# Kernel optimization log

Measured on AMD Instinct MI355X. Metric: run time of the kernel, lower is better.

The kernel has to match this reference:

```python
import jax, jax.numpy as jnp
import numpy as np

B, D, H = 16384, 1024, 1024
EPS = 1e-07


def setup_inputs() -> dict:
    key = jax.random.key(0)
    ks = jax.random.split(key, 16)
    s = 1.0 / np.sqrt(D)  # xavier-ish scale keeps exp() gate bounded
    mat = lambda k: (jax.random.normal(k, (D, H), dtype=jnp.float32) * s)
    zeros = lambda: jnp.zeros((H,), dtype=jnp.float32)
    return {
        "x": jax.random.normal(ks[0], (B, D), dtype=jnp.float32),
        "h_prev": jax.random.normal(ks[1], (B, H), dtype=jnp.float32) * 0.1,
        "c_prev": jax.random.normal(ks[2], (B, H), dtype=jnp.float32) * 0.1,
        "n_prev": jnp.ones((B, H), dtype=jnp.float32),
        "Wz": mat(ks[3]), "bWz": zeros(), "Rz": mat(ks[4]), "bRz": zeros(), "bz": zeros(),
        "Wi": mat(ks[5]), "bWi": zeros(), "Ri": mat(ks[6]), "bRi": zeros(), "bi": zeros(),
        "Wf": mat(ks[7]), "bWf": zeros(), "Rf": mat(ks[8]), "bRf": zeros(), "bf": zeros(),
        "Wo": mat(ks[9]), "bWo": zeros(), "Ro": mat(ks[10]), "bRo": zeros(), "bo": zeros(),
        "Wy": mat(ks[11]), "by": jnp.zeros((D,), dtype=jnp.float32),
    }


def reference(x, h_prev, c_prev, n_prev,
              Wz, bWz, Rz, bRz, bz,
              Wi, bWi, Ri, bRi, bi,
              Wf, bWf, Rf, bRf, bf,
              Wo, bWo, Ro, bRo, bo,
              Wy, by):
    # pre-activations: two fused GEMMs via concatenated weights
    Wcat = jnp.concatenate([Wz, Wi, Wf, Wo], axis=1)      # [D, 4H]
    Rcat = jnp.concatenate([Rz, Ri, Rf, Ro], axis=1)      # [H, 4H]
    bcat = jnp.concatenate([bWz + bRz + bz, bWi + bRi + bi,
                            bWf + bRf + bf, bWo + bRo + bo])
    pre = x @ Wcat + h_prev @ Rcat + bcat                  # [B, 4H]
    pz, pi, pf, po = jnp.split(pre, 4, axis=1)
    zt = jnp.tanh(pz)
    it = jnp.exp(pi)
    ft = jax.nn.sigmoid(pf)
    ot = jax.nn.sigmoid(po)
    C = ft * c_prev + it * zt
    n = ft * n_prev + it
    h = ot * jnp.tanh(C / (n + EPS))
    y = h @ Wy + by
    return y, (h, C, n)
```

## Files before the change

### kernel.cpp

```cpp
#include <hip/hip_runtime.h>
#include <math.h>
#include <stdint.h>


typedef __attribute__((ext_vector_type(8))) short bf16x8;
typedef __attribute__((ext_vector_type(4))) float f32x4;

constexpr int Bsz = 16384;
constexpr int Dd  = 1024;
constexpr int Hh  = 1024;
constexpr float EPSv = 1e-7f;

__device__ __forceinline__ unsigned short f2bf(float f) {
    union { float f; uint32_t u; } v; v.f = f;
    uint32_t u = v.u + 0x7fffu + ((v.u >> 16) & 1u);
    return (unsigned short)(u >> 16);
}

__device__ __forceinline__ void gload16(const void* g, void* l) {
    __builtin_amdgcn_global_load_lds(
        (const __attribute__((address_space(1))) void*)g,
        (__attribute__((address_space(3))) void*)l, 16, 0, 0);
}

__device__ __forceinline__ float sigm_f(float x) { return 1.f / (1.f + __expf(-x)); }
__device__ __forceinline__ float tanh_f(float x) {
    const float ax = fabsf(x);
    const float t = __expf(-2.f * ax);
    const float r = (1.f - t) / (1.f + t);
    return copysignf(r, x);
}

#define DSR(d, a, o) asm volatile("ds_read_b128 %0, %1 offset:" o : "=v"(d) : "v"(a) : "memory")

struct CvtArgs {
    const float* x;
    const float* hp;
    unsigned short* abf;
    const float* src[9];
    const float* bptr[12];
    unsigned short* wt;
    unsigned short* wyt;
    float* bs;
};

__global__ __launch_bounds__(256)
void cvt_all(CvtArgs P)
{
    __shared__ float tile[64][65];
    const int bid = blockIdx.x;
    const int t = threadIdx.x;

    if (bid < 16384) {
        const int idx = bid * 256 + t;
        const int n = idx * 8;
        const int b = n >> 11, k = n & 2047;
        const float* s = (k < 1024) ? (P.x + (size_t)b * 1024 + k)
                                    : (P.hp + (size_t)b * 1024 + (k - 1024));
        const float4 v0 = *(const float4*)s;
        const float4 v1 = *(const float4*)(s + 4);
        union { unsigned short u[8]; uint4 v; } pk;
        pk.u[0] = f2bf(v0.x); pk.u[1] = f2bf(v0.y); pk.u[2] = f2bf(v0.z); pk.u[3] = f2bf(v0.w);
        pk.u[4] = f2bf(v1.x); pk.u[5] = f2bf(v1.y); pk.u[6] = f2bf(v1.z); pk.u[7] = f2bf(v1.w);
        *(uint4*)(P.abf + n) = pk.v;
        return;
    }
    if (bid >= 18688) {
        const int j = (bid - 18688) * 256 + t;
        P.bs[j]        = P.bptr[0][j] + P.bptr[1][j]  + P.bptr[2][j];
        P.bs[1024 + j] = P.bptr[3][j] + P.bptr[4][j]  + P.bptr[5][j];
        P.bs[2048 + j] = P.bptr[6][j] + P.bptr[7][j]  + P.bptr[8][j];
        P.bs[3072 + j] = P.bptr[9][j] + P.bptr[10][j] + P.bptr[11][j];
        return;
    }
    const int wb = bid - 16384;
    const int id = wb >> 8, sub = wb & 255;
    const float* __restrict__ src = P.src[id];
    const int kt = sub & 15, jt = sub >> 4;
    {
        const int lr = t >> 4, lc = (t & 15) * 4;
        #pragma unroll
        for (int rr = 0; rr < 64; rr += 16) {
            const float4 v = *(const float4*)(src + (size_t)(kt * 64 + rr + lr) * 1024 + jt * 64 + lc);
            tile[rr + lr][lc + 0] = v.x;
            tile[rr + lr][lc + 1] = v.y;
            tile[rr + lr][lc + 2] = v.z;
            tile[rr + lr][lc + 3] = v.w;
        }
    }
    __syncthreads();
    const int jl = t >> 2, kc = (t & 3) * 16;
    const int j = jt * 64 + jl;
    union { unsigned short u[16]; uint4 v[2]; } pk;
    #pragma unroll
    for (int q = 0; q < 16; ++q) pk.u[q] = f2bf(tile[kc + q][jl]);
    uint4* d;
    if (id == 8) {
        d = (uint4*)(P.wyt + (size_t)j * 1024 + kt * 64 + kc);
    } else {
        const int g = id >> 1, kbase = (id & 1) ? 1024 : 0;
        const int cp = (j & 15) | (g << 4) | ((j >> 4) << 6);
        d = (uint4*)(P.wt + (size_t)cp * 2048 + kbase + kt * 64 + kc);
    }
    d[0] = pk.v[0];
    d[1] = pk.v[1];
}


template<int LD, int NTK, int NTILES, class Epi>
__device__ void mfma_core(const unsigned short* __restrict__ Ag,
                          const unsigned short* __restrict__ Bg,
                          int m0base, int n0, int t,
                          unsigned short* lds, Epi epi)
{
    constexpr int TOT = NTK * NTILES;
    const int lane = t & 63, wid = t >> 6;
    const int wr = wid >> 2, wc = wid & 3;
    const int cl = lane & 15, hi = lane >> 4;
    const int Lb = (int)(size_t)(__attribute__((address_space(3))) unsigned short*)lds;
    const int rdA0 = Lb + (wr * 128 + cl) * 128 + ((hi ^ (cl & 7)) << 4);
    const int rdB0 = Lb + 65536 + (wc * 64 + cl) * 128 + ((hi ^ (cl & 7)) << 4);
    const int srow = t >> 3;
    const int schk = ((t & 7) ^ (srow & 7)) * 8;
    const int sdst = t * 16;
    char* const L = (char*)lds;

    auto stgA = [&](int f, int buf) {
        const int ot = f / NTK, kt = f % NTK;
        const unsigned short* g = Ag + (size_t)(m0base + ot * 256 + srow) * LD + kt * 64 + schk;
        char* d = L + buf * 32768 + sdst;
        gload16(g,                  d);
        gload16(g + (size_t) 64 * LD, d + 8192);
        gload16(g + (size_t)128 * LD, d + 16384);
        gload16(g + (size_t)192 * LD, d + 24576);
    };
    auto stgB = [&](int f, int buf) {
        const int kt = f % NTK;
        const unsigned short* g = Bg + (size_t)(n0 + srow) * LD + kt * 64 + schk;
        char* d = L + 65536 + buf * 32768 + sdst;
        gload16(g,                  d);
        gload16(g + (size_t) 64 * LD, d + 8192);
        gload16(g + (size_t)128 * LD, d + 16384);
        gload16(g + (size_t)192 * LD, d + 24576);
    };

    f32x4 acc[8][4];
    #pragma unroll
    for (int i = 0; i < 8; ++i)
        #pragma unroll
        for (int j = 0; j < 4; ++j) acc[i][j] = (f32x4)0.f;

    stgA(0, 0); stgB(0, 0); stgB(1, 1);

    int bA = 0, bB = 0;
    for (int f = 0; f < TOT; ++f) {
        const int f1 = (f + 1 < TOT) ? f + 1 : TOT - 1;
        const int f2 = (f + 2 < TOT) ? f + 2 : TOT - 1;
        const int bB2 = (bB >= 1) ? bB - 1 : 2;

        asm volatile("s_waitcnt vmcnt(4)" ::: "memory");
        __builtin_amdgcn_s_barrier();
        stgA(f1, bA ^ 1);
        stgB(f2, bB2);

        const int aof  = rdA0 + (bA << 15);
        const int bof  = rdB0 + (bB << 15);
        const int aof1 = aof ^ 64;
        const int bof1 = bof ^ 64;
        bf16x8 a0[8], b0[4], a1[8], b1[4];

        DSR(a0[0], aof, "0");     DSR(a0[1], aof, "2048");
        DSR(a0[2], aof, "4096");  DSR(a0[3], aof, "6144");
        DSR(a0[4], aof, "8192");  DSR(a0[5], aof, "10240");
        DSR(a0[6], aof, "12288"); DSR(a0[7], aof, "14336");
        DSR(b0[0], bof, "0");     DSR(b0[1], bof, "2048");
        DSR(b0[2], bof, "4096");  DSR(b0[3], bof, "6144");
        DSR(a1[0], aof1, "0");     DSR(a1[1], aof1, "2048");
        DSR(a1[2], aof1, "4096");  DSR(a1[3], aof1, "6144");
        DSR(a1[4], aof1, "8192");  DSR(a1[5], aof1, "10240");
        DSR(a1[6], aof1, "12288"); DSR(a1[7], aof1, "14336");

        asm volatile("s_waitcnt lgkmcnt(8)" ::: "memory");
        __builtin_amdgcn_sched_barrier(0);
        __builtin_amdgcn_s_setprio(1);
        #pragma unroll
        for (int mf = 0; mf < 8; ++mf)
            #pragma unroll
            for (int nf = 0; nf < 4; ++nf)
                acc[mf][nf] = __builtin_amdgcn_mfma_f32_16x16x32_bf16(a0[mf], b0[nf], acc[mf][nf], 0, 0, 0);

        DSR(b1[0], bof1, "0");    DSR(b1[1], bof1, "2048");
        DSR(b1[2], bof1, "4096"); DSR(b1[3], bof1, "6144");

        asm volatile("s_waitcnt lgkmcnt(0)" ::: "memory");
        __builtin_amdgcn_sched_barrier(0);
        #pragma unroll
        for (int mf = 0; mf < 8; ++mf)
            #pragma unroll
            for (int nf = 0; nf < 4; ++nf)
                acc[mf][nf] = __builtin_amdgcn_mfma_f32_16x16x32_bf16(a1[mf], b1[nf], acc[mf][nf], 0, 0, 0);
        __builtin_amdgcn_s_setprio(0);

        if ((f % NTK) == NTK - 1) {
            epi(f / NTK, acc);
            #pragma unroll
            for (int i = 0; i < 8; ++i)
                #pragma unroll
                for (int j = 0; j < 4; ++j) acc[i][j] = (f32x4)0.f;
        }
        bA ^= 1;
        bB = (bB == 2) ? 0 : bB + 1;
    }
    asm volatile("s_waitcnt vmcnt(0)" ::: "memory");
}

__global__ __launch_bounds__(512, 2)
void gemm_gates(const unsigned short* __restrict__ A, const unsigned short* __restrict__ WT,
                const float* __restrict__ bsum,
                const float* __restrict__ c_prev, const float* __restrict__ n_prev,
                float* __restrict__ out_h, float* __restrict__ out_C, float* __restrict__ out_n,
                unsigned short* __restrict__ h_bf)
{
    __shared__ unsigned short lds[81920];
    const int t = threadIdx.x;
    const int b = blockIdx.x;
    const int nb  = (b & 7) * 2 + (b >> 7);
    const int mb0 = ((b >> 3) & 15) * 4;
    const int m0base = mb0 * 256;
    const int n0 = nb * 256;

    const int lane = t & 63, wid = t >> 6;
    const int wr = wid >> 2, wc = wid & 3;
    const int cl = lane & 15, hi = lane >> 4;
    const int j_out = nb * 64 + wc * 16 + cl;
    const float bz_ = bsum[j_out];
    const float bi_ = bsum[1024 + j_out];
    const float bf_ = bsum[2048 + j_out];
    const float bo_ = bsum[3072 + j_out];

    auto epi = [&](int ot, f32x4 (&acc)[8][4]) {
        #pragma unroll
        for (int mf = 0; mf < 8; ++mf) {
            const int rb = m0base + ot * 256 + wr * 128 + mf * 16 + hi * 4;
            #pragma unroll
            for (int r = 0; r < 4; ++r) {
                const size_t idx = (size_t)(rb + r) * 1024 + j_out;
                const float pz = acc[mf][0][r] + bz_;
                const float pi = acc[mf][1][r] + bi_;
                const float pf = acc[mf][2][r] + bf_;
                const float po = acc[mf][3][r] + bo_;
                const float zt = tanh_f(pz);
                const float it = __expf(pi);
                const float ft = sigm_f(pf);
                const float ot_ = sigm_f(po);
                const float Cv = ft * c_prev[idx] + it * zt;
                const float nv = ft * n_prev[idx] + it;
                const float hv = ot_ * tanh_f(Cv / (nv + EPSv));
                __builtin_nontemporal_store(hv, &out_h[idx]);
                __builtin_nontemporal_store(Cv, &out_C[idx]);
                __builtin_nontemporal_store(nv, &out_n[idx]);
                h_bf[idx] = f2bf(hv);
            }
        }
    };

    mfma_core<2048, 32, 4>(A, WT, m0base, n0, t, lds, epi);
}

__global__ __launch_bounds__(512, 2)
void gemm_y(const unsigned short* __restrict__ A, const unsigned short* __restrict__ WyT,
            const float* __restrict__ by, float* __restrict__ y)
{
    __shared__ unsigned short lds[81920];
    const int t = threadIdx.x;
    const int b = blockIdx.x;
    const int nb = b & 3, mb = b >> 2;
    const int m0base = mb * 256, n0 = nb * 256;

    const int lane = t & 63, wid = t >> 6;
    const int wr = wid >> 2, wc = wid & 3;
    const int cl = lane & 15, hi = lane >> 4;

    auto epi = [&](int ot, f32x4 (&acc)[8][4]) {
        (void)ot;
        #pragma unroll
        for (int mf = 0; mf < 8; ++mf) {
            const int rb = m0base + wr * 128 + mf * 16 + hi * 4;
            #pragma unroll
            for (int nf = 0; nf < 4; ++nf) {
                const int c = n0 + wc * 64 + nf * 16 + cl;
                const float bc = by[c];
                #pragma unroll
                for (int r = 0; r < 4; ++r)
                    __builtin_nontemporal_store(acc[mf][nf][r] + bc, &y[(size_t)(rb + r) * 1024 + c]);
            }
        }
    };

    mfma_core<1024, 16, 1>(A, WyT, m0base, n0, t, lds, epi);
}


constexpr int FBM = 64, FBN = 64, FBK = 16, FPAD = 4;

__global__ __launch_bounds__(256)
void fb_gates(const float* __restrict__ x, const float* __restrict__ h_prev,
              const float* __restrict__ c_prev, const float* __restrict__ n_prev,
              const float* __restrict__ Wz, const float* __restrict__ Rz,
              const float* __restrict__ Wi, const float* __restrict__ Ri,
              const float* __restrict__ Wf, const float* __restrict__ Rf,
              const float* __restrict__ Wo, const float* __restrict__ Ro,
              const float* __restrict__ bWz, const float* __restrict__ bRz, const float* __restrict__ bz,
              const float* __restrict__ bWi, const float* __restrict__ bRi, const float* __restrict__ bi,
              const float* __restrict__ bWf, const float* __restrict__ bRf, const float* __restrict__ bf_,
              const float* __restrict__ bWo, const float* __restrict__ bRo, const float* __restrict__ bo,
              float* __restrict__ out_h, float* __restrict__ out_C, float* __restrict__ out_n)
{
    __shared__ float sA[FBK][FBM + FPAD];
    __shared__ float sB[4][FBK][FBN + FPAD];
    const int t = threadIdx.x;
    const int col_blk = blockIdx.x & 15, row_blk = blockIdx.x >> 4;
    const int row0 = row_blk * FBM, col0 = col_blk * FBN;
    const int tx = t & 15, ty = t >> 4;
    float acc[4][4][4];
    #pragma unroll
    for (int g = 0; g < 4; ++g)
        for (int i = 0; i < 4; ++i)
            for (int j = 0; j < 4; ++j) acc[g][i][j] = 0.f;
    const int ar = t >> 2, ak = (t & 3) * 4, wk = t >> 4, wcc = (t & 15) * 4;
    for (int phase = 0; phase < 2; ++phase) {
        const float* Am = phase ? h_prev : x;
        const float* W0 = phase ? Rz : Wz; const float* W1 = phase ? Ri : Wi;
        const float* W2 = phase ? Rf : Wf; const float* W3 = phase ? Ro : Wo;
        for (int k0 = 0; k0 < 1024; k0 += FBK) {
            __syncthreads();
            {
                const float4 v = *(const float4*)(Am + (size_t)(row0 + ar) * 1024 + k0 + ak);
                sA[ak + 0][ar] = v.x; sA[ak + 1][ar] = v.y;
                sA[ak + 2][ar] = v.z; sA[ak + 3][ar] = v.w;
            }
            *(float4*)&sB[0][wk][wcc] = *(const float4*)(W0 + (size_t)(k0 + wk) * 1024 + col0 + wcc);
            *(float4*)&sB[1][wk][wcc] = *(const float4*)(W1 + (size_t)(k0 + wk) * 1024 + col0 + wcc);
            *(float4*)&sB[2][wk][wcc] = *(const float4*)(W2 + (size_t)(k0 + wk) * 1024 + col0 + wcc);
            *(float4*)&sB[3][wk][wcc] = *(const float4*)(W3 + (size_t)(k0 + wk) * 1024 + col0 + wcc);
            __syncthreads();
            #pragma unroll
            for (int kk = 0; kk < FBK; ++kk) {
                float a[4], bb[4][4];
                *(float4*)a = *(const float4*)&sA[kk][ty * 4];
                *(float4*)&bb[0][0] = *(const float4*)&sB[0][kk][tx * 4];
                *(float4*)&bb[1][0] = *(const float4*)&sB[1][kk][tx * 4];
                *(float4*)&bb[2][0] = *(const float4*)&sB[2][kk][tx * 4];
                *(float4*)&bb[3][0] = *(const float4*)&sB[3][kk][tx * 4];
                #pragma unroll
                for (int g = 0; g < 4; ++g)
                    for (int i = 0; i < 4; ++i)
                        for (int j = 0; j < 4; ++j)
                            acc[g][i][j] += a[i] * bb[g][j];
            }
        }
    }
    #pragma unroll
    for (int i = 0; i < 4; ++i) {
        const int r = row0 + ty * 4 + i;
        #pragma unroll
        for (int j = 0; j < 4; ++j) {
            const int c = col0 + tx * 4 + j;
            const float pz = acc[0][i][j] + bWz[c] + bRz[c] + bz[c];
            const float pi = acc[1][i][j] + bWi[c] + bRi[c] + bi[c];
            const float pf = acc[2][i][j] + bWf[c] + bRf[c] + bf_[c];
            const float po = acc[3][i][j] + bWo[c] + bRo[c] + bo[c];
            const float zt = tanhf(pz);
            const float it = expf(pi);
            const float ft = 1.f / (1.f + expf(-pf));
            const float ot = 1.f / (1.f + expf(-po));
            const size_t idx = (size_t)r * Hh + c;
            const float Cv = ft * c_prev[idx] + it * zt;
            const float nv = ft * n_prev[idx] + it;
            out_h[idx] = ot * tanhf(Cv / (nv + EPSv));
            out_C[idx] = Cv;
            out_n[idx] = nv;
        }
    }
}

__global__ __launch_bounds__(256)
void fb_ygemm(const float* __restrict__ hmat, const float* __restrict__ Wy,
              const float* __restrict__ by, float* __restrict__ y)
{
    __shared__ float sA[FBK][FBM + FPAD];
    __shared__ float sB[FBK][FBN + FPAD];
    const int t = threadIdx.x;
    const int col_blk = blockIdx.x & 15, row_blk = blockIdx.x >> 4;
    const int row0 = row_blk * FBM, col0 = col_blk * FBN;
    const int tx = t & 15, ty = t >> 4;
    float acc[4][4];
    #pragma unroll
    for (int i = 0; i < 4; ++i)
        for (int j = 0; j < 4; ++j) acc[i][j] = 0.f;
    const int ar = t >> 2, ak = (t & 3) * 4, wk = t >> 4, wcc = (t & 15) * 4;
    for (int k0 = 0; k0 < 1024; k0 += FBK) {
        __syncthreads();
        {
            const float4 v = *(const float4*)(hmat + (size_t)(row0 + ar) * 1024 + k0 + ak);
            sA[ak + 0][ar] = v.x; sA[ak + 1][ar] = v.y;
            sA[ak + 2][ar] = v.z; sA[ak + 3][ar] = v.w;
        }
        *(float4*)&sB[wk][wcc] = *(const float4*)(Wy + (size_t)(k0 + wk) * 1024 + col0 + wcc);
        __syncthreads();
        #pragma unroll
        for (int kk = 0; kk < FBK; ++kk) {
            float a[4], bb[4];
            *(float4*)a = *(const float4*)&sA[kk][ty * 4];
            *(float4*)bb = *(const float4*)&sB[kk][tx * 4];
            #pragma unroll
            for (int i = 0; i < 4; ++i)
                for (int j = 0; j < 4; ++j)
                    acc[i][j] += a[i] * bb[j];
        }
    }
    #pragma unroll
    for (int i = 0; i < 4; ++i) {
        const int r = row0 + ty * 4 + i;
        #pragma unroll
        for (int j = 0; j < 4; ++j) {
            const int c = col0 + tx * 4 + j;
            y[(size_t)r * Dd + c] = acc[i][j] + by[c];
        }
    }
}


extern "C" void kernel_launch(void* const* d_in, const int* in_sizes, int n_in,
                              void* d_out, int out_size, void* d_ws, size_t ws_size,
                              hipStream_t stream) {
    const float* x      = (const float*)d_in[0];
    const float* h_prev = (const float*)d_in[1];
    const float* c_prev = (const float*)d_in[2];
    const float* n_prev = (const float*)d_in[3];
    const float* Wz  = (const float*)d_in[4];
    const float* bWz = (const float*)d_in[5];
    const float* Rz  = (const float*)d_in[6];
    const float* bRz = (const float*)d_in[7];
    const float* bz  = (const float*)d_in[8];
    const float* Wi  = (const float*)d_in[9];
    const float* bWi = (const float*)d_in[10];
    const float* Ri  = (const float*)d_in[11];
    const float* bRi = (const float*)d_in[12];
    const float* bi  = (const float*)d_in[13];
    const float* Wf  = (const float*)d_in[14];
    const float* bWf = (const float*)d_in[15];
    const float* Rf  = (const float*)d_in[16];
    const float* bRf = (const float*)d_in[17];
    const float* bf_ = (const float*)d_in[18];
    const float* Wo  = (const float*)d_in[19];
    const float* bWo = (const float*)d_in[20];
    const float* Ro  = (const float*)d_in[21];
    const float* bRo = (const float*)d_in[22];
    const float* bo  = (const float*)d_in[23];
    const float* Wy  = (const float*)d_in[24];
    const float* by  = (const float*)d_in[25];

    float* y     = (float*)d_out;
    float* out_h = y + (size_t)Bsz * Dd;
    float* out_C = out_h + (size_t)Bsz * Hh;
    float* out_n = out_C + (size_t)Bsz * Hh;

    const size_t OFF_A    = 0;
    const size_t OFF_WT   = 67108864;
    const size_t OFF_WYT  = 83886080;
    const size_t OFF_HBF  = 85983232;
    const size_t OFF_BS   = 119537664;
    const size_t WS_NEED  = 119554048;

    if (ws_size >= WS_NEED) {
        char* ws = (char*)d_ws;
        unsigned short* A_bf = (unsigned short*)(ws + OFF_A);
        unsigned short* WT   = (unsigned short*)(ws + OFF_WT);
        unsigned short* WyT  = (unsigned short*)(ws + OFF_WYT);
        unsigned short* h_bf = (unsigned short*)(ws + OFF_HBF);
        float* bsum          = (float*)(ws + OFF_BS);

        CvtArgs P;
        P.x = x; P.hp = h_prev; P.abf = A_bf;
        P.src[0] = Wz; P.src[1] = Rz; P.src[2] = Wi; P.src[3] = Ri;
        P.src[4] = Wf; P.src[5] = Rf; P.src[6] = Wo; P.src[7] = Ro; P.src[8] = Wy;
        P.bptr[0] = bWz; P.bptr[1] = bRz; P.bptr[2]  = bz;
        P.bptr[3] = bWi; P.bptr[4] = bRi; P.bptr[5]  = bi;
        P.bptr[6] = bWf; P.bptr[7] = bRf; P.bptr[8]  = bf_;
        P.bptr[9] = bWo; P.bptr[10] = bRo; P.bptr[11] = bo;
        P.wt = WT; P.wyt = WyT; P.bs = bsum;
        cvt_all<<<18692, 256, 0, stream>>>(P);

        gemm_gates<<<256, 512, 0, stream>>>(A_bf, WT, bsum, c_prev, n_prev,
                                            out_h, out_C, out_n, h_bf);
        gemm_y<<<256, 512, 0, stream>>>(h_bf, WyT, by, y);
    } else {
        dim3 block(256);
        dim3 grid((Bsz / FBM) * (Hh / FBN));
        fb_gates<<<grid, block, 0, stream>>>(x, h_prev, c_prev, n_prev,
                                             Wz, Rz, Wi, Ri, Wf, Rf, Wo, Ro,
                                             bWz, bRz, bz, bWi, bRi, bi,
                                             bWf, bRf, bf_, bWo, bRo, bo,
                                             out_h, out_C, out_n);
        fb_ygemm<<<grid, block, 0, stream>>>(out_h, Wy, by, y);
    }
}
```

Before: 418.8 us.

## Restructure MFMA main loop into 8-phase barrier-synced schedule with double-buffered LDS

Replaces the per-k-tile loop (A double-buffered, B triple-buffered, 160KB LDS) with an unrolled two-tile iteration split into eight phases. Each phase reads a quarter of the fragments, issues a half-tile global-to-LDS load, and runs 16 MFMAs between workgroup barriers. LDS shrinks to 128KB with plain double buffering for both A and B. The goal is finer interleaving of loads, LDS reads and MFMAs across waves, and lower LDS footprint. The cost is many more barriers per tile, and the epilogue now only checks odd tile indices, which assumes NTK is even.

New measurement: 411.1 us. No clear change (-1.8%).

```diff
diff --git a/kernel.cpp b/kernel.cpp
--- a/kernel.cpp
+++ b/kernel.cpp
@@ -32,6 +32,9 @@
 }
 
 #define DSR(d, a, o) asm volatile("ds_read_b128 %0, %1 offset:" o : "=v"(d) : "v"(a) : "memory")
+#define LGKM0() { asm volatile("s_waitcnt lgkmcnt(0)" ::: "memory"); __builtin_amdgcn_sched_barrier(0); }
+#define VMC(n)  { asm volatile("s_waitcnt vmcnt(" #n ")" ::: "memory"); __builtin_amdgcn_sched_barrier(0); }
+#define BAR()   __builtin_amdgcn_s_barrier()
 
 struct CvtArgs {
     const float* x;
@@ -108,41 +111,50 @@
 
 
 template<int LD, int NTK, int NTILES, class Epi>
-__device__ void mfma_core(const unsigned short* __restrict__ Ag,
-                          const unsigned short* __restrict__ Bg,
-                          int m0base, int n0, int t,
-                          unsigned short* lds, Epi epi)
+__device__ void mfma8(const unsigned short* __restrict__ Ag,
+                      const unsigned short* __restrict__ Bg,
+                      int m0base, int n0, int t,
+                      unsigned short* lds, Epi epi)
 {
     constexpr int TOT = NTK * NTILES;
+    constexpr int NI  = TOT / 2;
     const int lane = t & 63, wid = t >> 6;
     const int wr = wid >> 2, wc = wid & 3;
     const int cl = lane & 15, hi = lane >> 4;
     const int Lb = (int)(size_t)(__attribute__((address_space(3))) unsigned short*)lds;
-    const int rdA0 = Lb + (wr * 128 + cl) * 128 + ((hi ^ (cl & 7)) << 4);
-    const int rdB0 = Lb + 65536 + (wc * 64 + cl) * 128 + ((hi ^ (cl & 7)) << 4);
+    const int swz = ((hi ^ (cl & 7)) << 4);
+    const int aof0  = Lb + (wr * 128 + cl) * 128 + swz;
+    const int aof1  = aof0 + 32768;
+    const int aof0x = aof0 ^ 64;
+    const int aof1x = aof1 ^ 64;
+    const int bof0  = Lb + 65536 + (wc * 64 + cl) * 128 + swz;
+    const int bof1  = bof0 + 32768;
+    const int bof0x = bof0 ^ 64;
+    const int bof1x = bof1 ^ 64;
     const int srow = t >> 3;
     const int schk = ((t & 7) ^ (srow & 7)) * 8;
     const int sdst = t * 16;
     char* const L = (char*)lds;
 
-    auto stgA = [&](int f, int buf) {
-        const int ot = f / NTK, kt = f % NTK;
-        const unsigned short* g = Ag + (size_t)(m0base + ot * 256 + srow) * LD + kt * 64 + schk;
-        char* d = L + buf * 32768 + sdst;
-        gload16(g,                  d);
-        gload16(g + (size_t) 64 * LD, d + 8192);
-        gload16(g + (size_t)128 * LD, d + 16384);
-        gload16(g + (size_t)192 * LD, d + 24576);
-    };
-    auto stgB = [&](int f, int buf) {
-        const int kt = f % NTK;
-        const unsigned short* g = Bg + (size_t)(n0 + srow) * LD + kt * 64 + schk;
-        char* d = L + 65536 + buf * 32768 + sdst;
-        gload16(g,                  d);
-        gload16(g + (size_t) 64 * LD, d + 8192);
-        gload16(g + (size_t)128 * LD, d + 16384);
-        gload16(g + (size_t)192 * LD, d + 24576);
-    };
+#define STGAH(f, h, buf) { const int ot_ = (f) / NTK, kt_ = (f) % NTK; \
+    const unsigned short* g_ = Ag + (size_t)(m0base + ot_ * 256 + (h) * 128 + srow) * LD + kt_ * 64 + schk; \
+    char* d_ = L + (buf) * 32768 + (h) * 16384 + sdst; \
+    gload16(g_, d_); gload16(g_ + (size_t)64 * LD, d_ + 8192); }
+#define STGBH(f, h, buf) { const int kt_ = (f) % NTK; \
+    const unsigned short* g_ = Bg + (size_t)(n0 + (h) * 128 + srow) * LD + kt_ * 64 + schk; \
+    char* d_ = L + 65536 + (buf) * 32768 + (h) * 16384 + sdst; \
+    gload16(g_, d_); gload16(g_ + (size_t)64 * LD, d_ + 8192); }
+#define RDB(dst, bof) { DSR(dst[0], bof, "0"); DSR(dst[1], bof, "2048"); \
+    DSR(dst[2], bof, "4096"); DSR(dst[3], bof, "6144"); }
+#define RDA0(dst, aof) { DSR(dst[0], aof, "0"); DSR(dst[1], aof, "2048"); \
+    DSR(dst[2], aof, "4096"); DSR(dst[3], aof, "6144"); }
+#define RDA1(dst, aof) { DSR(dst[0], aof, "8192"); DSR(dst[1], aof, "10240"); \
+    DSR(dst[2], aof, "12288"); DSR(dst[3], aof, "14336"); }
+#define MM(mb, Arr, Brr) { __builtin_amdgcn_s_setprio(1); \
+    _Pragma("unroll") for (int mf = 0; mf < 4; ++mf) \
+    _Pragma("unroll") for (int nf = 0; nf < 4; ++nf) \
+        acc[(mb) + mf][nf] = __builtin_amdgcn_mfma_f32_16x16x32_bf16(Arr[mf], Brr[nf], acc[(mb) + mf][nf], 0, 0, 0); \
+    __builtin_amdgcn_s_setprio(0); }
 
     f32x4 acc[8][4];
     #pragma unroll
@@ -150,68 +162,79 @@
         #pragma unroll
         for (int j = 0; j < 4; ++j) acc[i][j] = (f32x4)0.f;
 
-    stgA(0, 0); stgB(0, 0); stgB(1, 1);
-
-    int bA = 0, bB = 0;
-    for (int f = 0; f < TOT; ++f) {
-        const int f1 = (f + 1 < TOT) ? f + 1 : TOT - 1;
-        const int f2 = (f + 2 < TOT) ? f + 2 : TOT - 1;
-        const int bB2 = (bB >= 1) ? bB - 1 : 2;
-
-        asm volatile("s_waitcnt vmcnt(4)" ::: "memory");
-        __builtin_amdgcn_s_barrier();
-        stgA(f1, bA ^ 1);
-        stgB(f2, bB2);
-
-        const int aof  = rdA0 + (bA << 15);
-        const int bof  = rdB0 + (bB << 15);
-        const int aof1 = aof ^ 64;
-        const int bof1 = bof ^ 64;
-        bf16x8 a0[8], b0[4], a1[8], b1[4];
-
-        DSR(a0[0], aof, "0");     DSR(a0[1], aof, "2048");
-        DSR(a0[2], aof, "4096");  DSR(a0[3], aof, "6144");
-        DSR(a0[4], aof, "8192");  DSR(a0[5], aof, "10240");
-        DSR(a0[6], aof, "12288"); DSR(a0[7], aof, "14336");
-        DSR(b0[0], bof, "0");     DSR(b0[1], bof, "2048");
-        DSR(b0[2], bof, "4096");  DSR(b0[3], bof, "6144");
-        DSR(a1[0], aof1, "0");     DSR(a1[1], aof1, "2048");
-        DSR(a1[2], aof1, "4096");  DSR(a1[3], aof1, "6144");
-        DSR(a1[4], aof1, "8192");  DSR(a1[5], aof1, "10240");
-        DSR(a1[6], aof1, "12288"); DSR(a1[7], aof1, "14336");
-
-        asm volatile("s_waitcnt lgkmcnt(8)" ::: "memory");
-        __builtin_amdgcn_sched_barrier(0);
-        __builtin_amdgcn_s_setprio(1);
-        #pragma unroll
-        for (int mf = 0; mf < 8; ++mf)
-            #pragma unroll
-            for (int nf = 0; nf < 4; ++nf)
-                acc[mf][nf] = __builtin_amdgcn_mfma_f32_16x16x32_bf16(a0[mf], b0[nf], acc[mf][nf], 0, 0, 0);
-
-        DSR(b1[0], bof1, "0");    DSR(b1[1], bof1, "2048");
-        DSR(b1[2], bof1, "4096"); DSR(b1[3], bof1, "6144");
-
-        asm volatile("s_waitcnt lgkmcnt(0)" ::: "memory");
-        __builtin_amdgcn_sched_barrier(0);
-        #pragma unroll
-        for (int mf = 0; mf < 8; ++mf)
-            #pragma unroll
-            for (int nf = 0; nf < 4; ++nf)
-                acc[mf][nf] = __builtin_amdgcn_mfma_f32_16x16x32_bf16(a1[mf], b1[nf], acc[mf][nf], 0, 0, 0);
-        __builtin_amdgcn_s_setprio(0);
-
-        if ((f % NTK) == NTK - 1) {
-            epi(f / NTK, acc);
+    STGAH(0, 0, 0); STGAH(0, 1, 0);
+    STGBH(0, 0, 0); STGBH(0, 1, 0);
+    STGBH(1, 0, 1); STGBH(1, 1, 1);
+    VMC(4);
+    BAR();
+
+    bf16x8 Br0[4], Br1[4], Ar[4];
+
+    for (int it = 0; it < NI; ++it) {
+        const int f1 = 2 * it + 1;
+        int t2 = 2 * it + 2; if (t2 > TOT - 1) t2 = TOT - 1;
+        int t3 = 2 * it + 3; if (t3 > TOT - 1) t3 = TOT - 1;
+
+        RDB(Br0, bof0); RDA0(Ar, aof0);
+        STGAH(f1, 0, 1);
+        BAR(); LGKM0();
+        MM(0, Ar, Br0);
+        BAR();
+        RDB(Br1, bof0x); RDA0(Ar, aof0x);
+        STGAH(f1, 1, 1);
+        BAR(); LGKM0();
+        MM(0, Ar, Br1);
+        BAR();
+        RDA1(Ar, aof0);
+        STGBH(t2, 0, 0);
+        BAR(); LGKM0();
+        MM(4, Ar, Br0);
+        BAR();
+        RDA1(Ar, aof0x);
+        STGBH(t2, 1, 0);
+        VMC(4);
+        BAR(); LGKM0();
+        MM(4, Ar, Br1);
+        BAR();
+
+        RDB(Br0, bof1); RDA0(Ar, aof1);
+        STGAH(t2, 0, 0);
+        BAR(); LGKM0();
+        MM(0, Ar, Br0);
+        BAR();
+        RDB(Br1, bof1x); RDA0(Ar, aof1x);
+        STGAH(t2, 1, 0);
+        BAR(); LGKM0();
+        MM(0, Ar, Br1);
+        BAR();
+        RDA1(Ar, aof1);
+        STGBH(t3, 0, 1);
+        BAR(); LGKM0();
+        MM(4, Ar, Br0);
+        BAR();
+        RDA1(Ar, aof1x);
+        STGBH(t3, 1, 1);
+        VMC(4);
+        BAR(); LGKM0();
+        MM(4, Ar, Br1);
+        BAR();
+
+        if ((f1 % NTK) == NTK - 1) {
+            epi(f1 / NTK, acc);
             #pragma unroll
             for (int i = 0; i < 8; ++i)
                 #pragma unroll
                 for (int j = 0; j < 4; ++j) acc[i][j] = (f32x4)0.f;
         }
-        bA ^= 1;
-        bB = (bB == 2) ? 0 : bB + 1;
     }
     asm volatile("s_waitcnt vmcnt(0)" ::: "memory");
+
+#undef STGAH
+#undef STGBH
+#undef RDB
+#undef RDA0
+#undef RDA1
+#undef MM
 }
 
 __global__ __launch_bounds__(512, 2)
@@ -221,7 +244,7 @@
                 float* __restrict__ out_h, float* __restrict__ out_C, float* __restrict__ out_n,
                 unsigned short* __restrict__ h_bf)
 {
-    __shared__ unsigned short lds[81920];
+    __shared__ unsigned short lds[65536];
     const int t = threadIdx.x;
     const int b = blockIdx.x;
     const int nb  = (b & 7) * 2 + (b >> 7);
@@ -264,14 +287,14 @@
         }
     };
 
-    mfma_core<2048, 32, 4>(A, WT, m0base, n0, t, lds, epi);
+    mfma8<2048, 32, 4>(A, WT, m0base, n0, t, lds, epi);
 }
 
 __global__ __launch_bounds__(512, 2)
 void gemm_y(const unsigned short* __restrict__ A, const unsigned short* __restrict__ WyT,
             const float* __restrict__ by, float* __restrict__ y)
 {
-    __shared__ unsigned short lds[81920];
+    __shared__ unsigned short lds[65536];
     const int t = threadIdx.x;
     const int b = blockIdx.x;
     const int nb = b & 3, mb = b >> 2;
@@ -297,7 +320,7 @@
         }
     };
 
-    mfma_core<1024, 16, 1>(A, WyT, m0base, n0, t, lds, epi);
+    mfma8<1024, 16, 1>(A, WyT, m0base, n0, t, lds, epi);
 }
 
 
```
